# Optimization experiments

Measured on AMD Instinct MI355X. Metric: run time of the kernel, lower is better.

The kernel has to match this reference:

```python
import jax, jax.numpy as jnp
import numpy as np

P = 1024  # n_prototypes
D = 512   # embed_dim
B = 65536 # batch
EPS = 1e-12  # torch F.normalize eps


def _l2_normalize(x):
    # matches torch.nn.functional.normalize(x, dim=-1): x / max(||x||, eps)
    n = jnp.linalg.norm(x, axis=-1, keepdims=True)
    return x / jnp.maximum(n, EPS)


def setup_inputs() -> dict:
    key = jax.random.key(0)
    k1, k2 = jax.random.split(key)
    query_emb = jax.random.normal(k1, (B, D), dtype=jnp.float32)
    centroid_emb = jax.random.normal(k2, (P, D), dtype=jnp.float32)
    return {"query_emb": query_emb, "centroid_emb": centroid_emb}


def reference(query_emb, centroid_emb):
    q = _l2_normalize(query_emb)           # (B, D)
    c = _l2_normalize(centroid_emb)        # (P, D)
    logits = jnp.einsum('bd,pd->bp', q, c) # (B, P) cosine similarities
    hard_assignment = jnp.argmax(logits, axis=-1)              # (B,)
    hard_one_hot = jax.nn.one_hot(hard_assignment, P, dtype=logits.dtype)
    soft = jax.nn.softmax(logits, axis=-1)                     # (B, P)
    # straight-through: forward value = hard one-hot, gradient flows via soft
    routing_probs = hard_one_hot + soft - jax.lax.stop_gradient(soft)
    context_emb = jnp.einsum('bp,pd->bd', routing_probs, centroid_emb)  # (B, D)
    return context_emb, hard_assignment, routing_probs
```

## Files before the change

kernel.cpp:

```cpp
#include <hip/hip_runtime.h>
#include <hip/hip_bf16.h>
#include <climits>
#include <cstdint>

#define NB 65536
#define NP 1024
#define ND 512

#define MARGIN 4e-3f

typedef _Float16 f16x8 __attribute__((ext_vector_type(8)));
typedef float    f32x4 __attribute__((ext_vector_type(4)));

__device__ inline void load_lds16(const void* g, void* l) {
    __builtin_amdgcn_global_load_lds(
        (const __attribute__((address_space(1))) void*)g,
        (__attribute__((address_space(3))) void*)l, 16, 0, 0);
}

__global__ void centroid_rnorm_kernel(const float* __restrict__ cent,
                                      float* __restrict__ rnorm) {
    const int row  = blockIdx.x * 4 + (threadIdx.x >> 6);
    const int lane = threadIdx.x & 63;
    const float4* cr = (const float4*)(cent + (size_t)row * ND);
    float4 a = cr[2 * lane];
    float4 b = cr[2 * lane + 1];
    float s = a.x * a.x + a.y * a.y + a.z * a.z + a.w * a.w
            + b.x * b.x + b.y * b.y + b.z * b.z + b.w * b.w;
#pragma unroll
    for (int off = 32; off > 0; off >>= 1)
        s += __shfl_down(s, off, 64);
    if (lane == 0)
        rnorm[row] = 1.0f / fmaxf(sqrtf(s), 1e-12f);
}

__global__ void convertQ_kernel(const float* __restrict__ Q,
                                _Float16* __restrict__ Qp) {
    const size_t t = (size_t)blockIdx.x * 256 + threadIdx.x;
    const size_t base = t * 8;
    const float4* s = (const float4*)(Q + base);
    float4 x0 = s[0], x1 = s[1];
    float xs[8] = {x0.x, x0.y, x0.z, x0.w, x1.x, x1.y, x1.z, x1.w};
    f16x8 hi;
#pragma unroll
    for (int i = 0; i < 8; ++i)
        hi[i] = (_Float16)xs[i];
    *(f16x8*)(Qp + base) = hi;
}

__global__ void convertC_kernel(const float* __restrict__ C,
                                _Float16* __restrict__ Cp) {
    const size_t t = (size_t)blockIdx.x * 256 + threadIdx.x;
    const size_t base = t * 8;
    const float4* s = (const float4*)(C + base);
    float4 x0 = s[0], x1 = s[1];
    float xs[8] = {x0.x, x0.y, x0.z, x0.w, x1.x, x1.y, x1.z, x1.w};
    f16x8 hi;
#pragma unroll
    for (int i = 0; i < 8; ++i)
        hi[i] = (_Float16)xs[i];
    *(f16x8*)(Cp + base) = hi;
}

__launch_bounds__(256)
__global__ void gemm_top2_kernel(const _Float16* __restrict__ Qp,
                                 const _Float16* __restrict__ Cp,
                                 const float* __restrict__ rnorm,
                                 float* __restrict__ pv1,
                                 int*   __restrict__ pi1,
                                 float* __restrict__ pv2) {
    __shared__ __align__(16) _Float16 a_s[128 * 64];
    __shared__ __align__(16) _Float16 b_s[128 * 64];

    const int tid  = threadIdx.x;
    const int wave = tid >> 6, lane = tid & 63;

    const int bid = blockIdx.x;
    const int x = bid & 7, j = bid >> 3;
    const int nb = j & 7;
    const int mb = (j >> 3) * 8 + x;
    const int mbase = mb * 128, nbase = nb * 128;

    const int wm = wave >> 1, wn = wave & 1;
    const int quad = lane >> 4, l15 = lane & 15;

    f32x4 acc[4][4] = {};

    const _Float16* aBase = Qp + (size_t)(mbase + (lane >> 3)) * 512 + ((lane & 7) << 3);
    const _Float16* bBase = Cp + (size_t)(nbase + (lane >> 3)) * 512 + ((lane & 7) << 3);
    _Float16* aDst = a_s + wave * 512;
    _Float16* bDst = b_s + wave * 512;

    for (int kc = 0; kc < 8; ++kc) {
        const int kv = kc << 6;
        __syncthreads();
#pragma unroll
        for (int it = 0; it < 4; ++it) {
            const int s8 = (it * 4 + wave) * 8;
            load_lds16(aBase + (size_t)s8 * 512 + kv, aDst + it * 2048);
            load_lds16(bBase + (size_t)s8 * 512 + kv, bDst + it * 2048);
        }
        __syncthreads();
#pragma unroll
        for (int kk = 0; kk < 64; kk += 32) {
            f16x8 af[4], bf[4];
#pragma unroll
            for (int mt = 0; mt < 4; ++mt)
                af[mt] = *(const f16x8*)&a_s[(wm * 64 + mt * 16 + l15) * 64 + kk + quad * 8];
#pragma unroll
            for (int nt = 0; nt < 4; ++nt)
                bf[nt] = *(const f16x8*)&b_s[(wn * 64 + nt * 16 + l15) * 64 + kk + quad * 8];
#pragma unroll
            for (int mt = 0; mt < 4; ++mt)
#pragma unroll
                for (int nt = 0; nt < 4; ++nt)
                    acc[mt][nt] = __builtin_amdgcn_mfma_f32_16x16x32_f16(
                        af[mt], bf[nt], acc[mt][nt], 0, 0, 0);
        }
    }

    __syncthreads();
    float* lv1 = (float*)a_s;
    int*   li1 = (int*)(lv1 + 256);
    float* lv2 = (float*)(li1 + 256);

    float rn[4];
#pragma unroll
    for (int nt = 0; nt < 4; ++nt)
        rn[nt] = rnorm[nbase + wn * 64 + nt * 16 + l15];

#pragma unroll
    for (int mt = 0; mt < 4; ++mt) {
#pragma unroll
        for (int r = 0; r < 4; ++r) {
            float v1 = -3.0e38f, v2 = -3.0e38f; int i1 = INT_MAX;
#pragma unroll
            for (int nt = 0; nt < 4; ++nt) {
                float v = acc[mt][nt][r] * rn[nt];
                int   c = nbase + wn * 64 + nt * 16 + l15;
                if (v > v1) { v2 = v1; v1 = v; i1 = c; }
                else { if (v > v2) v2 = v; if (v == v1 && c < i1) i1 = c; }
            }
#pragma unroll
            for (int mask = 1; mask < 16; mask <<= 1) {
                float ov1 = __shfl_xor(v1, mask, 64);
                int   oi1 = __shfl_xor(i1, mask, 64);
                float ov2 = __shfl_xor(v2, mask, 64);
                if (ov1 > v1) { v2 = fmaxf(v1, ov2); v1 = ov1; i1 = oi1; }
                else if (ov1 == v1) { v2 = v1; i1 = min(i1, oi1); }
                else { v2 = fmaxf(v2, ov1); }
            }
            if (l15 == 0) {
                int row = wm * 64 + mt * 16 + quad * 4 + r;
                lv1[row * 2 + wn] = v1;
                li1[row * 2 + wn] = i1;
                lv2[row * 2 + wn] = v2;
            }
        }
    }
    __syncthreads();
    if (tid < 128) {
        float v1 = lv1[tid * 2],     v2 = lv2[tid * 2];     int i1 = li1[tid * 2];
        float w1 = lv1[tid * 2 + 1], w2 = lv2[tid * 2 + 1]; int j1 = li1[tid * 2 + 1];
        float V1, V2; int I1;
        if (w1 > v1)       { V1 = w1; I1 = j1; V2 = fmaxf(v1, w2); }
        else if (w1 == v1) { V1 = v1; I1 = min(i1, j1); V2 = v1; }
        else               { V1 = v1; I1 = i1; V2 = fmaxf(v2, w1); }
        const size_t g = (size_t)(mbase + tid) * 8 + nb;
        pv1[g] = V1; pi1[g] = I1; pv2[g] = V2;
    }
}

__global__ void merge_kernel(const float* __restrict__ pv1,
                             const int*   __restrict__ pi1,
                             const float* __restrict__ pv2,
                             float* __restrict__ assign_out,
                             int* __restrict__ rlist, int* __restrict__ rcount) {
    const int row = blockIdx.x * 256 + threadIdx.x;
    float v1 = -3.0e38f, v2 = -3.0e38f; int i1 = INT_MAX;
    const size_t b = (size_t)row * 8;
#pragma unroll
    for (int n = 0; n < 8; ++n) {
        float a1 = pv1[b + n]; int ai = pi1[b + n]; float a2 = pv2[b + n];
        if (a1 > v1)       { v2 = fmaxf(v1, a2); v1 = a1; i1 = ai; }
        else if (a1 == v1) { v2 = v1; i1 = min(i1, ai); }
        else               { v2 = fmaxf(v2, a1); }
    }
    assign_out[row] = (float)i1;
    if (v1 - v2 < MARGIN) {
        int p = atomicAdd(rcount, 1);
        rlist[p] = row;
    }
}

__launch_bounds__(256)
__global__ void refine_kernel(const float* __restrict__ Q,
                              const float* __restrict__ C,
                              const float* __restrict__ rnorm,
                              const int* __restrict__ rlist,
                              const int* __restrict__ rcount,
                              float* __restrict__ assign_out) {
    __shared__ float wv[8];
    __shared__ int   wi[8];
    const int n = *rcount;
    const int wave = threadIdx.x >> 6, lane = threadIdx.x & 63;
    for (int it = blockIdx.x * 2; it < n; it += gridDim.x * 2) {
        const int rowA = rlist[it];
        const int rowB = rlist[(it + 1 < n) ? (it + 1) : it];
        const float4* qrA = (const float4*)(Q + (size_t)rowA * ND);
        const float4* qrB = (const float4*)(Q + (size_t)rowB * ND);
        float4 qa  = qrA[lane], qa2 = qrA[lane + 64];
        float4 qb  = qrB[lane], qb2 = qrB[lane + 64];
        float bestA = -3.0e38f, bestB = -3.0e38f;
        int   biA = INT_MAX,    biB = INT_MAX;
        for (int i = 0; i < 64; ++i) {
            const int p0 = i * 16 + wave * 4;
            float sA[4], sB[4];
#pragma unroll
            for (int jj = 0; jj < 4; ++jj) {
                const float4* cr = (const float4*)(C + (size_t)(p0 + jj) * ND);
                float4 b = cr[lane], b2 = cr[lane + 64];
                sA[jj] = qa.x * b.x + qa.y * b.y + qa.z * b.z + qa.w * b.w
                       + qa2.x * b2.x + qa2.y * b2.y + qa2.z * b2.z + qa2.w * b2.w;
                sB[jj] = qb.x * b.x + qb.y * b.y + qb.z * b.z + qb.w * b.w
                       + qb2.x * b2.x + qb2.y * b2.y + qb2.z * b2.z + qb2.w * b2.w;
            }
#pragma unroll
            for (int m = 1; m < 64; m <<= 1) {
#pragma unroll
                for (int jj = 0; jj < 4; ++jj) {
                    sA[jj] += __shfl_xor(sA[jj], m, 64);
                    sB[jj] += __shfl_xor(sB[jj], m, 64);
                }
            }
#pragma unroll
            for (int jj = 0; jj < 4; ++jj) {
                float rnv = rnorm[p0 + jj];
                float vA = sA[jj] * rnv, vB = sB[jj] * rnv;
                if (vA > bestA) { bestA = vA; biA = p0 + jj; }
                if (vB > bestB) { bestB = vB; biB = p0 + jj; }
            }
        }
        __syncthreads();
        if (lane == 0) {
            wv[wave] = bestA;     wi[wave] = biA;
            wv[4 + wave] = bestB; wi[4 + wave] = biB;
        }
        __syncthreads();
        if (threadIdx.x == 0) {
            float bv = wv[0]; int b0 = wi[0];
            for (int w = 1; w < 4; ++w)
                if (wv[w] > bv || (wv[w] == bv && wi[w] < b0)) { bv = wv[w]; b0 = wi[w]; }
            assign_out[rowA] = (float)b0;
        }
        if (threadIdx.x == 64) {
            float bv = wv[4]; int b0 = wi[4];
            for (int w = 5; w < 8; ++w)
                if (wv[w] > bv || (wv[w] == bv && wi[w] < b0)) { bv = wv[w]; b0 = wi[w]; }
            assign_out[rowB] = (float)b0;
        }
    }
}

__global__ void scatter_kernel(const float* __restrict__ cent,
                               const float* __restrict__ assign,
                               float* __restrict__ ctx,
                               float* __restrict__ routing) {
    const int q    = blockIdx.x * 2 + (threadIdx.x >> 7);
    const int lane = threadIdx.x & 127;
    const int ci   = (int)assign[q];
    const float4* src = (const float4*)(cent + (size_t)ci * ND);
    ((float4*)(ctx + (size_t)q * ND))[lane] = src[lane];
    float4 z1 = {0.f, 0.f, 0.f, 0.f};
    float4 z2 = {0.f, 0.f, 0.f, 0.f};
    if ((ci >> 2) == lane)        ((float*)&z1)[ci & 3] = 1.0f;
    if ((ci >> 2) == lane + 128)  ((float*)&z2)[ci & 3] = 1.0f;
    float4* rr = (float4*)(routing + (size_t)q * NP);
    rr[lane]       = z1;
    rr[lane + 128] = z2;
}

extern "C" void kernel_launch(void* const* d_in, const int* in_sizes, int n_in,
                              void* d_out, int out_size, void* d_ws, size_t ws_size,
                              hipStream_t stream) {
    const float* query = (const float*)d_in[0];
    const float* cent  = (const float*)d_in[1];

    float* out        = (float*)d_out;
    float* ctx        = out;
    float* assign_out = out + (size_t)NB * ND;
    float* routing    = assign_out + NB;

    char* scratch = (char*)routing;
    _Float16* Qp    = (_Float16*)(scratch);
    _Float16* Cp    = (_Float16*)(scratch + 67108864);
    float*    rnorm = (float*)   (scratch + 68157440);
    float*    pv1   = (float*)   (scratch + 68161536);
    int*      pi1   = (int*)     (scratch + 70258688);
    float*    pv2   = (float*)   (scratch + 72355840);
    int*      rlist = (int*)     (scratch + 74452992);
    int*      rcount= (int*)     (scratch + 74715136);

    hipMemsetAsync(rcount, 0, sizeof(int), stream);

    centroid_rnorm_kernel<<<NP / 4, 256, 0, stream>>>(cent, rnorm);
    convertC_kernel<<<NP * ND / 8 / 256, 256, 0, stream>>>(cent, Cp);
    convertQ_kernel<<<NB * (ND / 8) / 256, 256, 0, stream>>>(query, Qp);
    gemm_top2_kernel<<<4096, 256, 0, stream>>>(Qp, Cp, rnorm, pv1, pi1, pv2);
    merge_kernel<<<NB / 256, 256, 0, stream>>>(pv1, pi1, pv2, assign_out, rlist, rcount);
    refine_kernel<<<512, 256, 0, stream>>>(query, cent, rnorm, rlist, rcount, assign_out);
    scatter_kernel<<<NB / 2, 256, 0, stream>>>(cent, assign_out, ctx, routing);
}
```

Baseline: 741.6 us.

## Double-buffer LDS tiles and XOR-swizzle layout in the top-2 GEMM

The K loop now stages into two LDS buffers, so the global-to-LDS load for the next 64-wide K chunk is issued while MFMAs run on the current one. This drops one barrier per iteration. Columns are also XOR-swizzled by row when written and read, to cut LDS bank conflicts on the f16x8 fragment reads. The cost is double the LDS footprint per block (64KB), which may lower occupancy.

```diff
diff --git a/kernel.cpp b/kernel.cpp
--- a/kernel.cpp
+++ b/kernel.cpp
@@ -69,8 +69,8 @@
                                  float* __restrict__ pv1,
                                  int*   __restrict__ pi1,
                                  float* __restrict__ pv2) {
-    __shared__ __align__(16) _Float16 a_s[128 * 64];
-    __shared__ __align__(16) _Float16 b_s[128 * 64];
+    __shared__ __align__(16) _Float16 a_s[2][128 * 64];
+    __shared__ __align__(16) _Float16 b_s[2][128 * 64];
 
     const int tid  = threadIdx.x;
     const int wave = tid >> 6, lane = tid & 63;
@@ -86,30 +86,44 @@
 
     f32x4 acc[4][4] = {};
 
-    const _Float16* aBase = Qp + (size_t)(mbase + (lane >> 3)) * 512 + ((lane & 7) << 3);
-    const _Float16* bBase = Cp + (size_t)(nbase + (lane >> 3)) * 512 + ((lane & 7) << 3);
-    _Float16* aDst = a_s + wave * 512;
-    _Float16* bDst = b_s + wave * 512;
-
-    for (int kc = 0; kc < 8; ++kc) {
+    const int scol = (((lane & 7) ^ (lane >> 3)) << 3);
+    const _Float16* aBase = Qp + (size_t)(mbase + (lane >> 3)) * 512 + scol;
+    const _Float16* bBase = Cp + (size_t)(nbase + (lane >> 3)) * 512 + scol;
+
+    auto STAGE = [&](int kc, int buf) {
         const int kv = kc << 6;
-        __syncthreads();
+        _Float16* aD = a_s[buf] + wave * 512;
+        _Float16* bD = b_s[buf] + wave * 512;
 #pragma unroll
         for (int it = 0; it < 4; ++it) {
             const int s8 = (it * 4 + wave) * 8;
-            load_lds16(aBase + (size_t)s8 * 512 + kv, aDst + it * 2048);
-            load_lds16(bBase + (size_t)s8 * 512 + kv, bDst + it * 2048);
-        }
-        __syncthreads();
-#pragma unroll
-        for (int kk = 0; kk < 64; kk += 32) {
+            load_lds16(aBase + (size_t)s8 * 512 + kv, aD + it * 2048);
+            load_lds16(bBase + (size_t)s8 * 512 + kv, bD + it * 2048);
+        }
+    };
+
+    STAGE(0, 0);
+    __syncthreads();
+
+    const int sx = l15 & 7;
+
+#pragma unroll 1
+    for (int kc = 0; kc < 8; ++kc) {
+        const int cur = kc & 1;
+        if (kc < 7) STAGE(kc + 1, cur ^ 1);
+
+        const _Float16* As = a_s[cur];
+        const _Float16* Bs = b_s[cur];
+#pragma unroll
+        for (int kk2 = 0; kk2 < 2; ++kk2) {
+            const int slot = (((kk2 << 2) + quad) ^ sx) << 3;
             f16x8 af[4], bf[4];
 #pragma unroll
             for (int mt = 0; mt < 4; ++mt)
-                af[mt] = *(const f16x8*)&a_s[(wm * 64 + mt * 16 + l15) * 64 + kk + quad * 8];
+                af[mt] = *(const f16x8*)&As[(wm * 64 + mt * 16 + l15) * 64 + slot];
 #pragma unroll
             for (int nt = 0; nt < 4; ++nt)
-                bf[nt] = *(const f16x8*)&b_s[(wn * 64 + nt * 16 + l15) * 64 + kk + quad * 8];
+                bf[nt] = *(const f16x8*)&Bs[(wn * 64 + nt * 16 + l15) * 64 + slot];
 #pragma unroll
             for (int mt = 0; mt < 4; ++mt)
 #pragma unroll
@@ -117,9 +131,9 @@
                     acc[mt][nt] = __builtin_amdgcn_mfma_f32_16x16x32_f16(
                         af[mt], bf[nt], acc[mt][nt], 0, 0, 0);
         }
-    }
-
-    __syncthreads();
+        __syncthreads();
+    }
+
     float* lv1 = (float*)a_s;
     int*   li1 = (int*)(lv1 + 256);
     float* lv2 = (float*)(li1 + 256);
```

After: 746.0 us. No clear change (+0.6%).

## Restructure GEMM-top2 to keep full-K query tile in LDS, stream centroids from global

Applied to the files above, without the earlier changes.

The GEMM kernel now loads a 128-row query tile with the full K=512 into LDS once, using XOR swizzling to avoid bank conflicts. Each of 8 waves covers 128 centroids in two 64-wide chunks, reading centroid fragments straight from global/L2. Partial top-2 results go out per 64-centroid chunk (16 per row), and merge is widened to match. This removes the per-K-step barriers and the repeated query-tile reloads across the 8 column blocks, but adds 128KB of LDS per block and uncached global reads for B.

```diff
diff --git a/kernel.cpp b/kernel.cpp
--- a/kernel.cpp
+++ b/kernel.cpp
@@ -62,112 +62,92 @@
     *(f16x8*)(Cp + base) = hi;
 }
 
-__launch_bounds__(256)
+__launch_bounds__(512, 2)
 __global__ void gemm_top2_kernel(const _Float16* __restrict__ Qp,
                                  const _Float16* __restrict__ Cp,
                                  const float* __restrict__ rnorm,
                                  float* __restrict__ pv1,
                                  int*   __restrict__ pi1,
                                  float* __restrict__ pv2) {
-    __shared__ __align__(16) _Float16 a_s[128 * 64];
-    __shared__ __align__(16) _Float16 b_s[128 * 64];
+    __shared__ __align__(16) _Float16 a_s[128 * 512];
 
     const int tid  = threadIdx.x;
     const int wave = tid >> 6, lane = tid & 63;
-
-    const int bid = blockIdx.x;
-    const int x = bid & 7, j = bid >> 3;
-    const int nb = j & 7;
-    const int mb = (j >> 3) * 8 + x;
-    const int mbase = mb * 128, nbase = nb * 128;
-
-    const int wm = wave >> 1, wn = wave & 1;
     const int quad = lane >> 4, l15 = lane & 15;
 
-    f32x4 acc[4][4] = {};
-
-    const _Float16* aBase = Qp + (size_t)(mbase + (lane >> 3)) * 512 + ((lane & 7) << 3);
-    const _Float16* bBase = Cp + (size_t)(nbase + (lane >> 3)) * 512 + ((lane & 7) << 3);
-    _Float16* aDst = a_s + wave * 512;
-    _Float16* bDst = b_s + wave * 512;
-
-    for (int kc = 0; kc < 8; ++kc) {
-        const int kv = kc << 6;
-        __syncthreads();
-#pragma unroll
-        for (int it = 0; it < 4; ++it) {
-            const int s8 = (it * 4 + wave) * 8;
-            load_lds16(aBase + (size_t)s8 * 512 + kv, aDst + it * 2048);
-            load_lds16(bBase + (size_t)s8 * 512 + kv, bDst + it * 2048);
-        }
-        __syncthreads();
-#pragma unroll
-        for (int kk = 0; kk < 64; kk += 32) {
-            f16x8 af[4], bf[4];
-#pragma unroll
-            for (int mt = 0; mt < 4; ++mt)
-                af[mt] = *(const f16x8*)&a_s[(wm * 64 + mt * 16 + l15) * 64 + kk + quad * 8];
+    const int mbase = blockIdx.x * 128;
+
+    {
+        const _Float16* src = Qp + (size_t)(mbase + wave) * 512
+                                 + ((lane ^ (wave & 7)) << 3);
+        _Float16* dst = a_s + wave * 512;
+#pragma unroll
+        for (int rd = 0; rd < 16; ++rd)
+            load_lds16(src + (size_t)rd * 4096, dst + rd * 4096);
+    }
+    __syncthreads();
+
+#pragma unroll 1
+    for (int c = 0; c < 2; ++c) {
+        const int cbase = wave * 128 + c * 64;
+
+        f32x4 acc[8][4] = {};
+
+#pragma unroll 4
+        for (int kc = 0; kc < 16; ++kc) {
+            f16x8 bf[4];
 #pragma unroll
             for (int nt = 0; nt < 4; ++nt)
-                bf[nt] = *(const f16x8*)&b_s[(wn * 64 + nt * 16 + l15) * 64 + kk + quad * 8];
-#pragma unroll
-            for (int mt = 0; mt < 4; ++mt)
+                bf[nt] = *(const f16x8*)(Cp
+                    + (size_t)(cbase + nt * 16 + l15) * 512 + kc * 32 + quad * 8);
+            f16x8 af[8];
+#pragma unroll
+            for (int mt = 0; mt < 8; ++mt) {
+                const int row  = mt * 16 + l15;
+                const int slot = (kc * 4 + quad) ^ (l15 & 7);
+                af[mt] = *(const f16x8*)&a_s[row * 512 + slot * 8];
+            }
+#pragma unroll
+            for (int mt = 0; mt < 8; ++mt)
 #pragma unroll
                 for (int nt = 0; nt < 4; ++nt)
                     acc[mt][nt] = __builtin_amdgcn_mfma_f32_16x16x32_f16(
                         af[mt], bf[nt], acc[mt][nt], 0, 0, 0);
         }
-    }
-
-    __syncthreads();
-    float* lv1 = (float*)a_s;
-    int*   li1 = (int*)(lv1 + 256);
-    float* lv2 = (float*)(li1 + 256);
-
-    float rn[4];
-#pragma unroll
-    for (int nt = 0; nt < 4; ++nt)
-        rn[nt] = rnorm[nbase + wn * 64 + nt * 16 + l15];
-
-#pragma unroll
-    for (int mt = 0; mt < 4; ++mt) {
-#pragma unroll
-        for (int r = 0; r < 4; ++r) {
-            float v1 = -3.0e38f, v2 = -3.0e38f; int i1 = INT_MAX;
-#pragma unroll
-            for (int nt = 0; nt < 4; ++nt) {
-                float v = acc[mt][nt][r] * rn[nt];
-                int   c = nbase + wn * 64 + nt * 16 + l15;
-                if (v > v1) { v2 = v1; v1 = v; i1 = c; }
-                else { if (v > v2) v2 = v; if (v == v1 && c < i1) i1 = c; }
-            }
-#pragma unroll
-            for (int mask = 1; mask < 16; mask <<= 1) {
-                float ov1 = __shfl_xor(v1, mask, 64);
-                int   oi1 = __shfl_xor(i1, mask, 64);
-                float ov2 = __shfl_xor(v2, mask, 64);
-                if (ov1 > v1) { v2 = fmaxf(v1, ov2); v1 = ov1; i1 = oi1; }
-                else if (ov1 == v1) { v2 = v1; i1 = min(i1, oi1); }
-                else { v2 = fmaxf(v2, ov1); }
-            }
-            if (l15 == 0) {
-                int row = wm * 64 + mt * 16 + quad * 4 + r;
-                lv1[row * 2 + wn] = v1;
-                li1[row * 2 + wn] = i1;
-                lv2[row * 2 + wn] = v2;
-            }
-        }
-    }
-    __syncthreads();
-    if (tid < 128) {
-        float v1 = lv1[tid * 2],     v2 = lv2[tid * 2];     int i1 = li1[tid * 2];
-        float w1 = lv1[tid * 2 + 1], w2 = lv2[tid * 2 + 1]; int j1 = li1[tid * 2 + 1];
-        float V1, V2; int I1;
-        if (w1 > v1)       { V1 = w1; I1 = j1; V2 = fmaxf(v1, w2); }
-        else if (w1 == v1) { V1 = v1; I1 = min(i1, j1); V2 = v1; }
-        else               { V1 = v1; I1 = i1; V2 = fmaxf(v2, w1); }
-        const size_t g = (size_t)(mbase + tid) * 8 + nb;
-        pv1[g] = V1; pi1[g] = I1; pv2[g] = V2;
+
+        float rn[4];
+#pragma unroll
+        for (int nt = 0; nt < 4; ++nt)
+            rn[nt] = rnorm[cbase + nt * 16 + l15];
+
+#pragma unroll
+        for (int mt = 0; mt < 8; ++mt) {
+#pragma unroll
+            for (int r = 0; r < 4; ++r) {
+                float v1 = -3.0e38f, v2 = -3.0e38f; int i1 = INT_MAX;
+#pragma unroll
+                for (int nt = 0; nt < 4; ++nt) {
+                    float v = acc[mt][nt][r] * rn[nt];
+                    int   cc = cbase + nt * 16 + l15;
+                    if (v > v1) { v2 = v1; v1 = v; i1 = cc; }
+                    else { if (v > v2) v2 = v; if (v == v1 && cc < i1) i1 = cc; }
+                }
+#pragma unroll
+                for (int mask = 1; mask < 16; mask <<= 1) {
+                    float ov1 = __shfl_xor(v1, mask, 64);
+                    int   oi1 = __shfl_xor(i1, mask, 64);
+                    float ov2 = __shfl_xor(v2, mask, 64);
+                    if (ov1 > v1) { v2 = fmaxf(v1, ov2); v1 = ov1; i1 = oi1; }
+                    else if (ov1 == v1) { v2 = v1; i1 = min(i1, oi1); }
+                    else { v2 = fmaxf(v2, ov1); }
+                }
+                if (l15 == 0) {
+                    const int row = mbase + mt * 16 + quad * 4 + r;
+                    const size_t g = (size_t)row * 16 + (wave * 2 + c);
+                    pv1[g] = v1; pi1[g] = i1; pv2[g] = v2;
+                }
+            }
+        }
     }
 }
 
@@ -178,9 +158,9 @@
                              int* __restrict__ rlist, int* __restrict__ rcount) {
     const int row = blockIdx.x * 256 + threadIdx.x;
     float v1 = -3.0e38f, v2 = -3.0e38f; int i1 = INT_MAX;
-    const size_t b = (size_t)row * 8;
-#pragma unroll
-    for (int n = 0; n < 8; ++n) {
+    const size_t b = (size_t)row * 16;
+#pragma unroll
+    for (int n = 0; n < 16; ++n) {
         float a1 = pv1[b + n]; int ai = pi1[b + n]; float a2 = pv2[b + n];
         if (a1 > v1)       { v2 = fmaxf(v1, a2); v1 = a1; i1 = ai; }
         else if (a1 == v1) { v2 = v1; i1 = min(i1, ai); }
@@ -296,17 +276,17 @@
     _Float16* Cp    = (_Float16*)(scratch + 67108864);
     float*    rnorm = (float*)   (scratch + 68157440);
     float*    pv1   = (float*)   (scratch + 68161536);
-    int*      pi1   = (int*)     (scratch + 70258688);
-    float*    pv2   = (float*)   (scratch + 72355840);
-    int*      rlist = (int*)     (scratch + 74452992);
-    int*      rcount= (int*)     (scratch + 74715136);
+    int*      pi1   = (int*)     (scratch + 72355840);
+    float*    pv2   = (float*)   (scratch + 76550144);
+    int*      rlist = (int*)     (scratch + 80744448);
+    int*      rcount= (int*)     (scratch + 81006592);
 
     hipMemsetAsync(rcount, 0, sizeof(int), stream);
 
     centroid_rnorm_kernel<<<NP / 4, 256, 0, stream>>>(cent, rnorm);
     convertC_kernel<<<NP * ND / 8 / 256, 256, 0, stream>>>(cent, Cp);
     convertQ_kernel<<<NB * (ND / 8) / 256, 256, 0, stream>>>(query, Qp);
-    gemm_top2_kernel<<<4096, 256, 0, stream>>>(Qp, Cp, rnorm, pv1, pi1, pv2);
+    gemm_top2_kernel<<<512, 512, 0, stream>>>(Qp, Cp, rnorm, pv1, pi1, pv2);
     merge_kernel<<<NB / 256, 256, 0, stream>>>(pv1, pi1, pv2, assign_out, rlist, rcount);
     refine_kernel<<<512, 256, 0, stream>>>(query, cent, rnorm, rlist, rcount, assign_out);
     scatter_kernel<<<NB / 2, 256, 0, stream>>>(cent, assign_out, ctx, routing);
```

Measured after the change: 767.2 us. 3.5% more time.

## Fuse query fp32-to-fp16 conversion into GEMM tile loads with XOR-swizzled LDS

Applied to the files above, without the earlier changes.

Removes the separate convertQ pass and its fp16 scratch buffer. The GEMM now reads fp32 query rows directly into registers, prefetches the next K chunk, converts to fp16 and stores into LDS. Both A and B tiles use an XOR swizzle to cut LDS bank conflicts. This saves a full write and reread of the 64 MB fp16 copy. In exchange the GEMM reads twice the bytes of A per tile, re-reads the query once per N block (8 times), and uses more registers for the prefetch buffer.

```diff
diff --git a/kernel.cpp b/kernel.cpp
--- a/kernel.cpp
+++ b/kernel.cpp
@@ -34,20 +34,6 @@
         rnorm[row] = 1.0f / fmaxf(sqrtf(s), 1e-12f);
 }
 
-__global__ void convertQ_kernel(const float* __restrict__ Q,
-                                _Float16* __restrict__ Qp) {
-    const size_t t = (size_t)blockIdx.x * 256 + threadIdx.x;
-    const size_t base = t * 8;
-    const float4* s = (const float4*)(Q + base);
-    float4 x0 = s[0], x1 = s[1];
-    float xs[8] = {x0.x, x0.y, x0.z, x0.w, x1.x, x1.y, x1.z, x1.w};
-    f16x8 hi;
-#pragma unroll
-    for (int i = 0; i < 8; ++i)
-        hi[i] = (_Float16)xs[i];
-    *(f16x8*)(Qp + base) = hi;
-}
-
 __global__ void convertC_kernel(const float* __restrict__ C,
                                 _Float16* __restrict__ Cp) {
     const size_t t = (size_t)blockIdx.x * 256 + threadIdx.x;
@@ -63,7 +49,7 @@
 }
 
 __launch_bounds__(256)
-__global__ void gemm_top2_kernel(const _Float16* __restrict__ Qp,
+__global__ void gemm_top2_kernel(const float* __restrict__ query,
                                  const _Float16* __restrict__ Cp,
                                  const float* __restrict__ rnorm,
                                  float* __restrict__ pv1,
@@ -83,33 +69,69 @@
 
     const int wm = wave >> 1, wn = wave & 1;
     const int quad = lane >> 4, l15 = lane & 15;
+    const int sx = l15 & 7;
 
     f32x4 acc[4][4] = {};
 
-    const _Float16* aBase = Qp + (size_t)(mbase + (lane >> 3)) * 512 + ((lane & 7) << 3);
-    const _Float16* bBase = Cp + (size_t)(nbase + (lane >> 3)) * 512 + ((lane & 7) << 3);
-    _Float16* aDst = a_s + wave * 512;
+    const int baseRow = tid >> 3;
+    const int slotA   = tid & 7;
+    const float* aSrc[4];
+#pragma unroll
+    for (int seg = 0; seg < 4; ++seg) {
+        const int r = baseRow + seg * 32;
+        aSrc[seg] = query + (size_t)(mbase + r) * 512 + ((slotA ^ (r & 7)) << 3);
+    }
+
+    const int scol = (((lane & 7) ^ (lane >> 3)) << 3);
+    const _Float16* bBase = Cp + (size_t)(nbase + (lane >> 3)) * 512 + scol;
     _Float16* bDst = b_s + wave * 512;
 
+    float4 aq[4][2];
+#pragma unroll
+    for (int seg = 0; seg < 4; ++seg) {
+        const float4* s = (const float4*)(aSrc[seg]);
+        aq[seg][0] = s[0]; aq[seg][1] = s[1];
+    }
+
+#pragma unroll 1
     for (int kc = 0; kc < 8; ++kc) {
         const int kv = kc << 6;
         __syncthreads();
+
+#pragma unroll
+        for (int seg = 0; seg < 4; ++seg) {
+            const int r = baseRow + seg * 32;
+            f16x8 h;
+            h[0] = (_Float16)aq[seg][0].x; h[1] = (_Float16)aq[seg][0].y;
+            h[2] = (_Float16)aq[seg][0].z; h[3] = (_Float16)aq[seg][0].w;
+            h[4] = (_Float16)aq[seg][1].x; h[5] = (_Float16)aq[seg][1].y;
+            h[6] = (_Float16)aq[seg][1].z; h[7] = (_Float16)aq[seg][1].w;
+            *(f16x8*)&a_s[r * 64 + slotA * 8] = h;
+        }
 #pragma unroll
         for (int it = 0; it < 4; ++it) {
             const int s8 = (it * 4 + wave) * 8;
-            load_lds16(aBase + (size_t)s8 * 512 + kv, aDst + it * 2048);
             load_lds16(bBase + (size_t)s8 * 512 + kv, bDst + it * 2048);
         }
+        if (kc < 7) {
+#pragma unroll
+            for (int seg = 0; seg < 4; ++seg) {
+                const float4* s = (const float4*)(aSrc[seg] + kv + 64);
+                aq[seg][0] = s[0]; aq[seg][1] = s[1];
+            }
+        }
         __syncthreads();
-#pragma unroll
-        for (int kk = 0; kk < 64; kk += 32) {
+
+#pragma unroll
+        for (int kk2 = 0; kk2 < 2; ++kk2) {
+            const int slot = (((kk2 << 2) + quad) ^ sx) << 3;
             f16x8 af[4], bf[4];
 #pragma unroll
             for (int mt = 0; mt < 4; ++mt)
-                af[mt] = *(const f16x8*)&a_s[(wm * 64 + mt * 16 + l15) * 64 + kk + quad * 8];
+                af[mt] = *(const f16x8*)&a_s[(wm * 64 + mt * 16 + l15) * 64 + slot];
 #pragma unroll
             for (int nt = 0; nt < 4; ++nt)
-                bf[nt] = *(const f16x8*)&b_s[(wn * 64 + nt * 16 + l15) * 64 + kk + quad * 8];
+                bf[nt] = *(const f16x8*)&b_s[(wn * 64 + nt * 16 + l15) * 64 + slot];
 #pragma unroll
             for (int mt = 0; mt < 4; ++mt)
 #pragma unroll
@@ -292,21 +314,19 @@
     float* routing    = assign_out + NB;
 
     char* scratch = (char*)routing;
-    _Float16* Qp    = (_Float16*)(scratch);
-    _Float16* Cp    = (_Float16*)(scratch + 67108864);
-    float*    rnorm = (float*)   (scratch + 68157440);
-    float*    pv1   = (float*)   (scratch + 68161536);
-    int*      pi1   = (int*)     (scratch + 70258688);
-    float*    pv2   = (float*)   (scratch + 72355840);
-    int*      rlist = (int*)     (scratch + 74452992);
-    int*      rcount= (int*)     (scratch + 74715136);
+    _Float16* Cp    = (_Float16*)(scratch);
+    float*    rnorm = (float*)   (scratch + 1048576);
+    float*    pv1   = (float*)   (scratch + 1052672);
+    int*      pi1   = (int*)     (scratch + 3149824);
+    float*    pv2   = (float*)   (scratch + 5246976);
+    int*      rlist = (int*)     (scratch + 7344128);
+    int*      rcount= (int*)     (scratch + 7606272);
 
     hipMemsetAsync(rcount, 0, sizeof(int), stream);
 
     centroid_rnorm_kernel<<<NP / 4, 256, 0, stream>>>(cent, rnorm);
     convertC_kernel<<<NP * ND / 8 / 256, 256, 0, stream>>>(cent, Cp);
-    convertQ_kernel<<<NB * (ND / 8) / 256, 256, 0, stream>>>(query, Qp);
-    gemm_top2_kernel<<<4096, 256, 0, stream>>>(Qp, Cp, rnorm, pv1, pi1, pv2);
+    gemm_top2_kernel<<<4096, 256, 0, stream>>>(query, Cp, rnorm, pv1, pi1, pv2);
     merge_kernel<<<NB / 256, 256, 0, stream>>>(pv1, pi1, pv2, assign_out, rlist, rcount);
     refine_kernel<<<512, 256, 0, stream>>>(query, cent, rnorm, rlist, rcount, assign_out);
     scatter_kernel<<<NB / 2, 256, 0, stream>>>(cent, assign_out, ctx, routing);
```

Result: no change. 750.8 us (+1.2%).
